# Kernel optimization log

Hardware: AMD Instinct MI355X
Metric: run time of the kernel (lower is better)

## Reference

```python
import jax, jax.numpy as jnp
import numpy as np

# model dims
B, L, D, K = 4, 1024, 512, 24      # batch, seq_len, d_model, num_eigh
KU, KY, NL, DT = 3, 2, 4, 512      # ar depth u, ar depth y, num_layers, d_target
EPS = 1e-5


def _hankel_eigh():
    # Hankel matrix Z[i,j] = 2 / ((i+j)^3 - (i+j)), i,j in 1..L; top-K eigenpairs
    idx = np.arange(1, L + 1, dtype=np.float64)
    s = idx[:, None] + idx[None, :]
    Z = 2.0 / (s ** 3 - s)
    vals, vecs = np.linalg.eigh(Z)  # ascending
    return (jnp.asarray(vals[-K:], jnp.float32),       # [K]
            jnp.asarray(vecs[:, -K:], jnp.float32))    # [L, K]


def setup_inputs() -> dict:
    key = jax.random.key(0)
    ks = jax.random.split(key, 12)
    sc = 1.0 / np.sqrt(D)
    eig_vals, eig_vecs = _hankel_eigh()
    return {
        "inputs": jax.random.normal(ks[0], (B, L, D), jnp.float32),
        "emb_w": jax.random.normal(ks[1], (D, D), jnp.float32) * sc,
        "emb_b": jnp.zeros((D,), jnp.float32),
        "ln_scale": jnp.ones((NL, D), jnp.float32),
        "ln_bias": jnp.zeros((NL, D), jnp.float32),
        "m_y": jax.random.normal(ks[2], (NL, D, KY, D), jnp.float32) * 0.02,
        "m_u": jax.random.normal(ks[3], (NL, D, D, KU), jnp.float32) * sc,
        "m_phi": jax.random.normal(ks[4], (NL, D * K, D), jnp.float32) * 0.02,
        "w1": jax.random.normal(ks[5], (NL, D, 2 * D), jnp.float32) * sc,
        "b1": jnp.zeros((NL, 2 * D), jnp.float32),
        "proj_w": jax.random.normal(ks[6], (D, DT), jnp.float32) * sc,
        "proj_b": jnp.zeros((DT,), jnp.float32),
        "eig_vals": eig_vals,
        "eig_vecs": eig_vecs,
    }


def _layer_norm(x, s, b):
    mu = jnp.mean(x, axis=-1, keepdims=True)
    var = jnp.mean(jnp.square(x - mu), axis=-1, keepdims=True)
    return (x - mu) * jax.lax.rsqrt(var + EPS) * s + b


def _stu(x, m_y_l, m_u_l, m_phi_l, eig_vals, eig_vecs):
    # x: [B, L, D]
    n = 2 * L
    U = jnp.fft.rfft(x, n=n, axis=1)                 # [B, nf, D]
    V = jnp.fft.rfft(eig_vecs, n=n, axis=0)          # [nf, K]
    # causal conv of each eigvec filter with each channel -> x_tilde [B, L, K, D]
    xt = jnp.fft.irfft(U[:, :, None, :] * V[None, :, :, None], n=n, axis=1)[:, :L]
    xt = xt * (eig_vals[None, None, :, None] ** 0.25)
    delta_phi = xt.reshape(B, L, K * D) @ m_phi_l    # [B, L, D]
    ar = jnp.zeros_like(delta_phi)
    for i in range(KU):
        c = jnp.einsum('bli,oi->blo', x, m_u_l[:, :, i])
        if i > 0:
            c = jnp.pad(c, ((0, 0), (i, 0), (0, 0)))[:, :L]
        ar = ar + c
    deltas = delta_phi + ar
    # y_t = sum_{j<KY} m_y[:,j,:] @ y_{t-1-j} + delta_t  (sequential recurrence)
    def step(carry, d_t):                            # carry [B, KY, D], d_t [B, D]
        y = jnp.einsum('okd,bkd->bo', m_y_l, carry) + d_t
        carry = jnp.concatenate([y[:, None, :], carry[:, :-1]], axis=1)
        return carry, y
    _, ys = jax.lax.scan(step, jnp.zeros((B, KY, D), x.dtype),
                         jnp.transpose(deltas, (1, 0, 2)))
    return jnp.transpose(ys, (1, 0, 2))              # [B, L, D]


def reference(inputs, emb_w, emb_b, ln_scale, ln_bias, m_y, m_u, m_phi,
              w1, b1, proj_w, proj_b, eig_vals, eig_vecs):
    x = inputs @ emb_w + emb_b
    for l in range(NL):
        z = x
        h = _layer_norm(x, ln_scale[l], ln_bias[l])
        h = _stu(h, m_y[l], m_u[l], m_phi[l], eig_vals, eig_vecs)
        h = jax.nn.gelu(h, approximate=False)        # torch GELU default (erf)
        g = h @ w1[l] + b1[l]
        a, b = jnp.split(g, 2, axis=-1)
        h = a * jax.nn.sigmoid(b)                    # GLU(dim=-1)
        x = h + z                                    # residual (dropout=0, eval)
    return x @ proj_w + proj_b
```

## Files before the change

### kernel.cpp

```cpp
#include <hip/hip_runtime.h>
#include <math.h>

typedef __bf16 bf;
typedef __attribute__((ext_vector_type(4))) __bf16 bfv4;
typedef __attribute__((ext_vector_type(8))) __bf16 bfv8;
typedef __attribute__((ext_vector_type(4))) float f32x4;

__device__ __forceinline__ void gload16(const void* g, void* l) {
  __builtin_amdgcn_global_load_lds((const __attribute__((address_space(1))) void*)g,
                                   (__attribute__((address_space(3))) void*)l, 16, 0, 0);
}

struct GOp {
  const bf* A; long la, lKa, lMa, sAz; int zshA, kzA;
  const bf* B; long lb, lKb, sBz; int zmskB, kzB;
  float* C; long ldc, sCz;
  bf* Cb; long ldcb, sCbz;
  const float* bias; int K, maskCmp, mBlk, spS;
};

template<int tB,int tF32,int tB16,int tMASK,int tACC>
__device__ __forceinline__ void gbody(const GOp g, int z, long m0, long n0,
                                      bf* lsA, bf* lsB, const bf* zpg) {
  const int t = threadIdx.x;
  const bf* Ap = g.A + (long)(z >> g.zshA) * g.sAz;
  const bf* Bp = g.B + (long)(z & g.zmskB) * g.sBz;
  const int w = t >> 6, l = t & 63;
  const int wm = (w >> 1) * 64, wn = (w & 1) * 64;
  const int lr = l & 15, lk = (l >> 4) * 8;
  const int r0 = t >> 2, ko = (t & 3) * 8;
  const long rowA1 = m0 + r0, rowA2 = rowA1 + 64;
  const long baseA1 = (rowA1 >> 9) * g.lMa + (rowA1 & 511) * g.la;
  const long baseA2 = (rowA2 >> 9) * g.lMa + (rowA2 & 511) * g.la;
  const long baseB1 = (n0 + r0) * g.lb;
  const int zbA = z * g.kzA, zbB = z * g.kzB;
  const int ct = ((int)rowA1 + 1) & 7;
  const long convB = (long)ct * 2065 + 1023 - (long)rowA1;
  f32x4 acc[4][4];
  #pragma unroll
  for (int i = 0; i < 4; i++)
    #pragma unroll
    for (int j = 0; j < 4; j++) acc[i][j] = (f32x4){0.f, 0.f, 0.f, 0.f};

  for (int k0 = 0; k0 < g.K; k0 += 32) {
    const int kk = k0 + ko;
    const int bA = (kk >> 9) + zbA, bB = (kk >> 9) + zbB;
    const long kb = (long)bB * g.lKb + (kk & 511);
    const bf* ga; const bf* ga2;
    if (tMASK == 3) {
      ga  = Ap + convB + kk;
      ga2 = ga - 64;
    } else {
      const long ka = (long)bA * g.lKa + (kk & 511);
      ga  = Ap + baseA1 + ka;
      ga2 = Ap + baseA2 + ka;
      if (tMASK == 1) { if ((int)(rowA1 & 15) < bA) { ga = zpg; ga2 = zpg; } }
      if (tMASK == 2) { if ((int)(rowA1 & 63) < g.maskCmp) { ga = zpg; ga2 = zpg; } }
    }
    const bf* gb = Bp + baseB1 + kb;
    gload16(ga,             &lsA[t * 8]);
    gload16(ga2,            &lsA[2048 + t * 8]);
    gload16(gb,             &lsB[t * 8]);
    gload16(gb + 64 * g.lb, &lsB[2048 + t * 8]);
    __syncthreads();
    bfv8 av[4], bv[4];
    #pragma unroll
    for (int i = 0; i < 4; i++) av[i] = *(const bfv8*)&lsA[(wm + i * 16 + lr) * 32 + lk];
    #pragma unroll
    for (int i = 0; i < 4; i++) bv[i] = *(const bfv8*)&lsB[(wn + i * 16 + lr) * 32 + lk];
    #pragma unroll
    for (int i = 0; i < 4; i++)
      #pragma unroll
      for (int j = 0; j < 4; j++)
        acc[i][j] = __builtin_amdgcn_mfma_f32_16x16x32_bf16(av[i], bv[j], acc[i][j], 0, 0, 0);
    __syncthreads();
  }
  const int orow = (l >> 4) * 4, ocol = lr;
  #pragma unroll
  for (int i = 0; i < 4; i++)
    #pragma unroll
    for (int j = 0; j < 4; j++) {
      long col = n0 + wn + j * 16 + ocol;
      float bb = tB ? g.bias[col] : 0.f;
      #pragma unroll
      for (int r = 0; r < 4; r++) {
        long row = m0 + wm + i * 16 + orow + r;
        float v = acc[i][j][r] + bb;
        if (tF32) {
          long idx = (long)z * g.sCz + row * g.ldc + col;
          if (tACC) v += g.C[idx];
          g.C[idx] = v;
        }
        if (tB16) g.Cb[(long)z * g.sCbz + row * g.ldcb + col] = (bf)v;
      }
    }
}

template<int tB,int tF32,int tB16,int tMASK,int tACC,int tSPEC=0,
         int sB=0,int sF32=0,int sB16=0,int sMASK=0,int sACC=0>
__global__ __launch_bounds__(256) void gemm_k(GOp g, GOp gx, GOp gy, int Zmain,
                                              const bf* __restrict__ zpg) {
  __shared__ bf lsA[4096], lsB[4096];
  int z = blockIdx.z;
  if (tSPEC && z >= Zmain) {
    int flat = (z - Zmain) * (int)(gridDim.x * gridDim.y)
             + (int)blockIdx.y * (int)gridDim.x + (int)blockIdx.x;
    if (flat >= gx.mBlk) return;
    int zz = flat >> 6, t64 = flat & 63;
    long m0 = (long)(t64 >> 3) * 128, n0 = (long)(t64 & 7) * 128;
    if (zz < gx.spS) gbody<sB,sF32,sB16,sMASK,sACC>(gx, zz, m0, n0, lsA, lsB, zpg);
    else             gbody<sB,sF32,sB16,sMASK,sACC>(gy, 0,  m0, n0, lsA, lsB, zpg);
  } else {
    gbody<tB,tF32,tB16,tMASK,tACC>(g, z, (long)blockIdx.x * 128, (long)blockIdx.y * 128,
                                   lsA, lsB, zpg);
  }
}

static inline GOp mkop(const void* A, long la, long lKa, long lMa, long sAz, int zshA, int kzA,
                       const void* B, long lb, long lKb, long sBz, int zmskB, int kzB,
                       void* C, long ldc, long sCz, void* Cb, long ldcb, long sCbz,
                       const void* bias, int K) {
  GOp g;
  g.A = (const bf*)A; g.la = la; g.lKa = lKa; g.lMa = lMa; g.sAz = sAz; g.zshA = zshA; g.kzA = kzA;
  g.B = (const bf*)B; g.lb = lb; g.lKb = lKb; g.sBz = sBz; g.zmskB = zmskB; g.kzB = kzB;
  g.C = (float*)C; g.ldc = ldc; g.sCz = sCz;
  g.Cb = (bf*)Cb; g.ldcb = ldcb; g.sCbz = sCbz;
  g.bias = (const float*)bias; g.K = K; g.maskCmp = 0; g.mBlk = 0; g.spS = 0;
  return g;
}

template<int tB,int tF32,int tB16,int tMASK,int tACC,int tSPEC=0,
         int sB=0,int sF32=0,int sB16=0,int sMASK=0,int sACC=0>
static inline void LG(hipStream_t st, int gx_, int gy_, int gz_, const GOp& g,
                      const GOp& gsx, const GOp& gsy, int Zmain, const bf* zpg) {
  gemm_k<tB,tF32,tB16,tMASK,tACC,tSPEC,sB,sF32,sB16,sMASK,sACC>
      <<<dim3(gx_, gy_, gz_), 256, 0, st>>>(g, gsx, gsy, Zmain, zpg);
}


template<typename TI, typename TO>
__global__ __launch_bounds__(256) void k_trt(const TI* __restrict__ in, TO* __restrict__ out,
                                             long ldin, long inz, long ldout, long outz) {
  __shared__ float tile[64][65];
  int z = blockIdx.z;
  int c0 = blockIdx.x * 64, r0 = blockIdx.y * 64;
  int tx = threadIdx.x & 63, ty = threadIdx.x >> 6;
  #pragma unroll
  for (int i = ty; i < 64; i += 4) tile[i][tx] = (float)in[(long)z * inz + (long)(c0 + i) * ldin + r0 + tx];
  __syncthreads();
  #pragma unroll
  for (int i = ty; i < 64; i += 4) out[(long)z * outz + (long)(r0 + i) * ldout + c0 + tx] = (TO)tile[tx][i];
}

__global__ __launch_bounds__(256) void k_trtS(const float* __restrict__ in, bf* __restrict__ out,
                                              long ldin, long ldout, const float* __restrict__ scl) {
  __shared__ float tile[64][65];
  int c0 = blockIdx.x * 64, r0 = blockIdx.y * 64;
  int tx = threadIdx.x & 63, ty = threadIdx.x >> 6;
  #pragma unroll
  for (int i = ty; i < 64; i += 4) tile[i][tx] = in[(long)(c0 + i) * ldin + r0 + tx];
  __syncthreads();
  float sc = scl[(c0 + tx) >> 9];
  #pragma unroll
  for (int i = ty; i < 64; i += 4) out[(long)(r0 + i) * ldout + c0 + tx] = (bf)(tile[tx][i] * sc);
}

__global__ void k_scl(const float* __restrict__ evals, float* __restrict__ scl) {
  int k = threadIdx.x;
  if (k < 24) scl[k] = powf(evals[k], 0.25f);
}

__global__ void k_pvec(const float* __restrict__ evecs, bf* __restrict__ out) {
  long id = (long)blockIdx.x * 256 + threadIdx.x;
  if (id >= 24L * 16512) return;
  int kf = (int)(id / 16512);
  int rem = (int)(id % 16512);
  int c = rem / 2064, j = rem % 2064;
  int d = j - c;
  float v = (d >= 0 && d <= 1023) ? evecs[(long)(1023 - d) * 24 + kf] : 0.f;
  out[id] = (bf)v;
}

__global__ void k_mut(const float* __restrict__ mul_, bf* __restrict__ out) {
  long id = (long)blockIdx.x * 256 + threadIdx.x;
  long r = id >> 9; int d = (int)(id & 511);
  int i = (int)(r >> 9), o = (int)(r & 511);
  out[id] = (bf)mul_[(long)o * 1536 + d * 3 + i];
}

__global__ __launch_bounds__(256) void k_prep(const float* __restrict__ myl,
                                              bf* __restrict__ cmpow, bf* __restrict__ trs) {
  __shared__ float t[64][65];
  long bid = blockIdx.x;
  if (bid < 10240) {
    long id = bid * 256 + threadIdx.x;
    if (id < 2097152) {
      int half = (int)(id >> 20);
      int r = (int)(id & 1048575);
      int p = r >> 10, q = r & 1023;
      float v;
      if (half == 0) v = (p == q) ? 1.f : 0.f;
      else if (p < 512) v = myl[(long)p * 1024 + q];
      else v = (q == p - 512) ? 1.f : 0.f;
      cmpow[id] = (bf)v;
    } else if (id < 2621440) {
      long id2 = id - 2097152;
      int x = (int)(id2 >> 9), y = (int)(id2 & 511);
      trs[(long)x * 1024 + 512 + y] = (bf)((x == y) ? 1.f : 0.f);
    }
  } else {
    int tile = (int)(bid - 10240);
    int txx = tile >> 3, tyy = tile & 7;
    int lx = threadIdx.x & 63, ly = threadIdx.x >> 6;
    #pragma unroll
    for (int i = ly; i < 64; i += 4)
      t[i][lx] = myl[(long)(tyy * 64 + i) * 1024 + txx * 64 + lx];
    __syncthreads();
    #pragma unroll
    for (int i = ly; i < 64; i += 4)
      trs[(long)(txx * 64 + i) * 1024 + tyy * 64 + lx] = (bf)t[lx][i];
  }
}

__global__ __launch_bounds__(256) void k_ln(const float* __restrict__ x, const float* __restrict__ sc,
                                            const float* __restrict__ bi, bf* __restrict__ hb) {
  __shared__ float red[8];
  long row = blockIdx.x;
  const float* xr = x + row * 512;
  int t = threadIdx.x;
  float a = xr[t], b2 = xr[t + 256];
  float s = a + b2;
  #pragma unroll
  for (int o = 32; o; o >>= 1) s += __shfl_down(s, o, 64);
  if ((t & 63) == 0) red[t >> 6] = s;
  __syncthreads();
  float mu = (red[0] + red[1] + red[2] + red[3]) * (1.f / 512.f);
  __syncthreads();
  float c1 = a - mu, c2 = b2 - mu;
  float qq = c1 * c1 + c2 * c2;
  #pragma unroll
  for (int o = 32; o; o >>= 1) qq += __shfl_down(qq, o, 64);
  if ((t & 63) == 0) red[t >> 6] = qq;
  __syncthreads();
  float var = (red[0] + red[1] + red[2] + red[3]) * (1.f / 512.f);
  float rs = rsqrtf(var + 1e-5f);
  hb[row * 512 + t]       = (bf)(c1 * rs * sc[t] + bi[t]);
  hb[row * 512 + t + 256] = (bf)(c2 * rs * sc[t + 256] + bi[t + 256]);
}

__global__ void k_deltasS(const float* __restrict__ dp, long stride, int S,
                          const bf* __restrict__ callb, bf* __restrict__ db) {
  long id = (long)blockIdx.x * 256 + threadIdx.x;
  int o = (int)(id & 511); long row = id >> 9; int tt = (int)(row & 1023);
  float v = 0.f;
  for (int zz = 0; zz < S; ++zz) v += dp[(long)zz * stride + id];
  for (int i = 0; i < 3; ++i)
    if (tt >= i) v += (float)callb[(row - i) * 1536 + i * 512 + o];
  db[id] = (bf)v;
}

__global__ void k_egather(const float* __restrict__ dp, long stride, int S,
                          float* __restrict__ E, bf* __restrict__ eb0) {
  long id = (long)blockIdx.x * 256 + threadIdx.x;
  int p = (int)(id & 1023); long r = id >> 10;
  int b = (int)(r >> 6), c = (int)(r & 63);
  int tq = c * 16 + ((p < 512) ? 15 : 14);
  long idx = ((long)(b << 10) + tq) * 512 + (p & 511);
  float v = 0.f;
  for (int zz = 0; zz < S; ++zz) v += dp[(long)zz * stride + idx];
  E[id] = v; eb0[id] = (bf)v;
}

__global__ void k_sfinal(const float* __restrict__ E, bf* __restrict__ ssb) {
  long id = (long)blockIdx.x * 256 + threadIdx.x;
  int c = (int)((id >> 10) & 63);
  ssb[id] = (c > 0) ? (bf)E[id - 1024] : (bf)0.f;
}

__global__ void k_combgelu(const float* __restrict__ dp, long stride, int S,
                           const bf* __restrict__ outh, bf* __restrict__ yg) {
  long id = (long)blockIdx.x * 256 + threadIdx.x;
  int o = (int)(id & 511); long row = id >> 9;
  int b = (int)(row >> 10), tt = (int)(row & 1023);
  int c = tt >> 4, j = tt & 15;
  long wv = ((long)(j * 512 + o)) * 256 + b * 64 + c;
  float v = (float)outh[wv];
  for (int zz = 0; zz < S; ++zz) v += dp[(long)zz * stride + id];
  yg[id] = (bf)(0.5f * v * (1.f + erff(v * 0.70710678118654752f)));
}

__global__ void k_glures(const bf* __restrict__ g, float* __restrict__ x) {
  long id = (long)blockIdx.x * 256 + threadIdx.x;
  int o = (int)(id & 511); long row = id >> 9;
  float a = (float)g[row * 1024 + o], bb = (float)g[row * 1024 + 512 + o];
  x[id] = x[id] + a / (1.f + expf(-bb));
}

__global__ void k_cast(const float* __restrict__ in, bf* __restrict__ out, long n4) {
  long id = (long)blockIdx.x * 256 + threadIdx.x;
  if (id >= n4) return;
  float4 v = *(const float4*)(in + id * 4);
  bfv4 o; o[0] = (bf)v.x; o[1] = (bf)v.y; o[2] = (bf)v.z; o[3] = (bf)v.w;
  *(bfv4*)(out + id * 4) = o;
}

__global__ void k_fill(float* p, long n, float v) {
  long id = (long)blockIdx.x * 256 + threadIdx.x;
  if (id < n) p[id] = v;
}

struct Lay {
  long ZPG, SSTB, SCL, EMBT, PROJT, PVEC, CMPOW, TRS, WU, X, MPHITL, MUTL, W1TL,
       HB, HTB, DSLOT, DP, RC, E, EB0, EB1, need;
  int nk, S;
};
static Lay mkLay(int nk, int S) {
  Lay L; long o = 0;
  auto al = [&](long sz) { long r = o; o += (sz + 255) & ~255L; return r; };
  L.nk = nk; L.S = S;
  L.ZPG   = al(4096);
  L.SSTB  = al(524288);
  L.SCL   = al(256);
  L.EMBT  = al(524288);
  L.PROJT = al(524288);
  L.PVEC  = al(24L * 16512 * 2);
  L.CMPOW = al(17L * 2097152);
  L.TRS   = al(2L * 2097152);
  L.WU    = al(8388608);
  L.X     = al(8388608);
  L.MPHITL= al(12582912);
  L.MUTL  = al(1572864);
  L.W1TL  = al(1048576);
  L.HB    = al(4194304);
  L.HTB   = al(4194304);
  L.DSLOT = al(4194304);
  L.DP    = al((long)S * 8388608);
  long rc = (long)nk * 4194304;
  if (rc < 16777216) rc = 16777216;
  L.RC    = al(rc);
  L.E     = al(1048576);
  L.EB0   = al(524288);
  L.EB1   = al(524288);
  L.need  = o;
  return L;
}

extern "C" void kernel_launch(void* const* d_in, const int* in_sizes, int n_in,
                              void* d_out, int out_size, void* d_ws, size_t ws_size,
                              hipStream_t stream) {
  Lay L = mkLay(12, 4);
  if (L.need > (long)ws_size) L = mkLay(8, 4);
  if (L.need > (long)ws_size) L = mkLay(4, 2);
  if (L.need > (long)ws_size) {
    k_fill<<<8192, 256, 0, stream>>>((float*)d_out, 2097152, 1.0e6f + (float)(ws_size >> 20));
    return;
  }
  const float* inp  = (const float*)d_in[0];
  const float* embw = (const float*)d_in[1];
  const float* embb = (const float*)d_in[2];
  const float* lns  = (const float*)d_in[3];
  const float* lnb  = (const float*)d_in[4];
  const float* m_y  = (const float*)d_in[5];
  const float* m_u  = (const float*)d_in[6];
  const float* mphi = (const float*)d_in[7];
  const float* w1   = (const float*)d_in[8];
  const float* b1   = (const float*)d_in[9];
  const float* pw   = (const float*)d_in[10];
  const float* pb   = (const float*)d_in[11];
  const float* evals = (const float*)d_in[12];
  const float* evecs = (const float*)d_in[13];

  char* w = (char*)d_ws;
  bf*    ZPG   = (bf*)(w + L.ZPG);
  bf*    SSTB  = (bf*)(w + L.SSTB);
  float* SCL   = (float*)(w + L.SCL);
  bf*    EMBT  = (bf*)(w + L.EMBT);
  bf*    PROJT = (bf*)(w + L.PROJT);
  bf*    PVEC  = (bf*)(w + L.PVEC);
  bf*    CMPOW = (bf*)(w + L.CMPOW);
  bf*    TRSa  = (bf*)(w + L.TRS);
  bf*    TRSb  = TRSa + 1048576;
  bf*    WUa   = (bf*)(w + L.WU);
  bf*    WUb   = (bf*)(w + L.WU + 4194304);
  float* X     = (float*)(w + L.X);
  bf*    MPHITL= (bf*)(w + L.MPHITL);
  bf*    MUTL  = (bf*)(w + L.MUTL);
  bf*    W1TL  = (bf*)(w + L.W1TL);
  bf*    HB    = (bf*)(w + L.HB);
  bf*    HTB   = (bf*)(w + L.HTB);
  bf*    DELTAB= (bf*)(w + L.DSLOT);
  bf*    YGB   = (bf*)(w + L.DSLOT);
  float* DP    = (float*)(w + L.DP);
  bf*    XTC   = (bf*)(w + L.RC);
  bf*    CALLB = (bf*)(w + L.RC);
  bf*    OUTH  = (bf*)(w + L.RC + 12582912);
  bf*    G     = (bf*)(w + L.RC);
  float* E     = (float*)(w + L.E);
  bf*    EB0   = (bf*)(w + L.EB0);
  bf*    EB1   = (bf*)(w + L.EB1);
  bf*    INB   = HB;
  hipStream_t st = stream;
  const int nk = L.nk, S = L.S, nchunk = 24 / nk;
  const long DPS = 2097152;
  const int Kcphi = nk * 512 / S, kzphi = Kcphi >> 9;
  const int Kcy = 8192 / S, kzy = Kcy >> 9;
  GOp gnull = {};
  const int BIGZ = 1 << 30;

  hipMemsetAsync(w + L.ZPG, 0, 4096, st);

  k_scl<<<1, 32, 0, st>>>(evals, SCL);
  k_pvec<<<1549, 256, 0, st>>>(evecs, PVEC);
  k_trt<float, bf><<<dim3(8, 8, 1), 256, 0, st>>>(embw, EMBT, 512, 0, 512, 0);
  k_trt<float, bf><<<dim3(8, 8, 1), 256, 0, st>>>(pw, PROJT, 512, 0, 512, 0);
  k_cast<<<2048, 256, 0, st>>>(inp, INB, 524288);
  LG<1,1,0,0,0>(st, 32, 4, 1,
      mkop(INB, 512, 512, 262144, 0, 30, 0, EMBT, 512, 512, 0, 0, 0,
           X, 512, 0, nullptr, 0, 0, embb, 512), gnull, gnull, BIGZ, ZPG);

  for (int l = 0; l < 4; ++l) {
    k_prep<<<10368, 256, 0, st>>>(m_y + (long)l * 524288, CMPOW, TRSa);
    k_trtS<<<dim3(192, 8, 1), 256, 0, st>>>(mphi + (long)l * 6291456, MPHITL, 512, 12288, SCL);
    k_mut<<<3072, 256, 0, st>>>(m_u + (long)l * 786432, MUTL);
    k_trt<float, bf><<<dim3(8, 16, 1), 256, 0, st>>>(w1 + (long)l * 524288, W1TL, 1024, 0, 512, 0);

    k_ln<<<4096, 256, 0, st>>>(X, lns + l * 512, lnb + l * 512, HB);
    k_trt<bf, bf><<<dim3(16, 8, 4), 256, 0, st>>>(HB, HTB, 512, 524288, 1024, 524288);

    int hostRound = 0;
    for (int kc = 0; kc < nchunk; ++kc) {
      GOp gconv = mkop(PVEC + (long)kc * nk * 16512, 0, 0, 0, 16512, 2, 0,
                       HTB, 1024, 512, 524288, 3, 0,
                       nullptr, 0, 0, XTC, 512, 524288, nullptr, 1024);
      if (hostRound < 4) {
        int s = 1 << hostRound;
        bf* TRScur = (hostRound & 1) ? TRSb : TRSa;
        bf* TRSnxt = (hostRound & 1) ? TRSa : TRSb;
        GOp dx = mkop(CMPOW + 1048576, 1024, 512, 524288, 1048576, 0, 0,
                      TRScur, 1024, 512, 0, 0, 0,
                      nullptr, 0, 0, CMPOW + (long)(s + 1) * 1048576, 1024, 1048576,
                      nullptr, 1024);
        dx.mBlk = 64 * (s + 1); dx.spS = s;
        GOp dy = mkop(TRScur, 1024, 512, 524288, 0, 0, 0,
                      CMPOW + (long)s * 1048576, 1024, 512, 0, 0, 0,
                      nullptr, 0, 0, TRSnxt, 1024, 0, nullptr, 1024);
        int nzs = (64 * (s + 1) + 31) / 32;
        LG<0,0,1,3,0, 1, 0,0,1,0,0>(st, 8, 4, 4 * nk + nzs, gconv, dx, dy, 4 * nk, ZPG);
        ++hostRound;
      } else {
        LG<0,0,1,3,0>(st, 8, 4, 4 * nk, gconv, gnull, gnull, BIGZ, ZPG);
      }
      GOp gphi = mkop(XTC, 512, 2097152, 262144, 0, 30, kzphi,
                      MPHITL + (long)kc * nk * 512, 12288, 512, 0, 0, kzphi,
                      DP, 512, DPS, nullptr, 0, 0, nullptr, Kcphi);
      if (hostRound < 4) {
        int s = 1 << hostRound;
        bf* TRScur = (hostRound & 1) ? TRSb : TRSa;
        bf* TRSnxt = (hostRound & 1) ? TRSa : TRSb;
        GOp dx = mkop(CMPOW + 1048576, 1024, 512, 524288, 1048576, 0, 0,
                      TRScur, 1024, 512, 0, 0, 0,
                      nullptr, 0, 0, CMPOW + (long)(s + 1) * 1048576, 1024, 1048576,
                      nullptr, 1024);
        dx.mBlk = 64 * (s + 1); dx.spS = s;
        GOp dy = mkop(TRScur, 1024, 512, 524288, 0, 0, 0,
                      CMPOW + (long)s * 1048576, 1024, 512, 0, 0, 0,
                      nullptr, 0, 0, TRSnxt, 1024, 0, nullptr, 1024);
        int nzs = (64 * (s + 1) + 127) / 128;
        if (kc == 0) LG<0,1,0,0,0, 1, 0,0,1,0,0>(st, 32, 4, S + nzs, gphi, dx, dy, S, ZPG);
        else         LG<0,1,0,0,1, 1, 0,0,1,0,0>(st, 32, 4, S + nzs, gphi, dx, dy, S, ZPG);
        ++hostRound;
      } else {
        if (kc == 0) LG<0,1,0,0,0>(st, 32, 4, S, gphi, gnull, gnull, BIGZ, ZPG);
        else         LG<0,1,0,0,1>(st, 32, 4, S, gphi, gnull, gnull, BIGZ, ZPG);
      }
    }

    LG<0,0,1,0,0>(st, 32, 12, 1,
        mkop(HB, 512, 512, 262144, 0, 30, 0, MUTL, 512, 512, 0, 0, 0,
             nullptr, 0, 0, CALLB, 1536, 0, nullptr, 512), gnull, gnull, BIGZ, ZPG);
    k_deltasS<<<8192, 256, 0, st>>>(DP, DPS, S, CALLB, DELTAB);

    LG<0,1,0,1,0>(st, 32, 4, S,
        mkop(DELTAB, 512, -512, 262144, 0, 30, kzy,
             CMPOW, 1024, 1048576, 0, 0, kzy,
             DP, 512, DPS, nullptr, 0, 0, nullptr, Kcy), gnull, gnull, BIGZ, ZPG);

    k_egather<<<1024, 256, 0, st>>>(DP, DPS, S, E, EB0);
    const bf* Wc = CMPOW + 16L * 1048576;
    const bf* Uc = TRSa;
    bf* EBc = EB0; bf* EBn = EB1;
    bf* WUn = WUa;
    for (int k = 1; k <= 5; ++k) {
      int sh = 1 << (k - 1);
      GOp mn = mkop(Wc, 1024, 512, 524288, (long)(Uc - Wc), 0, 0,
                    Uc, 1024, 512, (long)(Wc - Uc), 1, 0,
                    nullptr, 0, 0, WUn, 1024, 1048576, nullptr, 1024);
      GOp sp = mkop(EBc - (long)sh * 1024, 1024, 512, 524288, 0, 30, 0,
                    Wc, 1024, 512, 0, 0, 0,
                    E, 1024, 0, EBn, 1024, 0, nullptr, 1024);
      sp.maskCmp = sh; sp.mBlk = 16; sp.spS = 99;
      LG<0,0,1,0,0, 1, 0,1,1,2,1>(st, 8, 8, 3, mn, sp, gnull, 2, ZPG);
      Wc = WUn; Uc = WUn + 1048576;
      WUn = (k & 1) ? WUb : WUa;
      bf* tmp = EBc; EBc = EBn; EBn = tmp;
    }
    GOp fe = mkop(EBc - 32L * 1024, 1024, 512, 524288, 0, 30, 0,
                  Wc, 1024, 512, 0, 0, 0,
                  E, 1024, 0, nullptr, 0, 0, nullptr, 1024);
    fe.maskCmp = 32;
    LG<0,1,0,2,1>(st, 2, 8, 1, fe, gnull, gnull, BIGZ, ZPG);
    k_sfinal<<<1024, 256, 0, st>>>(E, SSTB);

    LG<0,0,1,0,0>(st, 64, 2, 1,
        mkop(CMPOW + 1048576, 1024, 512, 1048576, 0, 30, 0,
             SSTB, 1024, 512, 0, 0, 0,
             nullptr, 0, 0, OUTH, 256, 0, nullptr, 1024), gnull, gnull, BIGZ, ZPG);
    k_combgelu<<<8192, 256, 0, st>>>(DP, DPS, S, OUTH, YGB);
    LG<1,0,1,0,0>(st, 32, 8, 1,
        mkop(YGB, 512, 512, 262144, 0, 30, 0, W1TL, 512, 512, 0, 0, 0,
             nullptr, 0, 0, G, 1024, 0, b1 + (long)l * 1024, 512), gnull, gnull, BIGZ, ZPG);
    k_glures<<<8192, 256, 0, st>>>(G, X);
  }

  k_cast<<<2048, 256, 0, st>>>(X, INB, 524288);
  LG<1,1,0,0,0>(st, 32, 4, 1,
      mkop(INB, 512, 512, 262144, 0, 30, 0, PROJT, 512, 512, 0, 0, 0,
           (float*)d_out, 512, 0, nullptr, 0, 0, pb, 512), gnull, gnull, BIGZ, ZPG);
}
```

Before: 2.986 ms.

## Store only the top half of companion-matrix powers and trim triangular conv K-loop

Companion matrix powers are now stored as 512-row top halves (PTOP) with negative strides instead of full 1024x1024 blocks, because the bottom half is a shifted copy of the previous power. This halves both the power-doubling GEMM work and the memory traffic for the prep kernel. The Toeplitz conv GEMM (mask 3) now stops its K loop at m0+128, skipping the zero upper triangle. The last doubling step also drops the unused W-power grid slice. Together these rework the indexing across several GEMMs, so any addressing mistake would give wrong results.

```diff
diff --git a/kernel.cpp b/kernel.cpp
--- a/kernel.cpp
+++ b/kernel.cpp
@@ -36,13 +36,14 @@
   const int zbA = z * g.kzA, zbB = z * g.kzB;
   const int ct = ((int)rowA1 + 1) & 7;
   const long convB = (long)ct * 2065 + 1023 - (long)rowA1;
+  const int Kend = (tMASK == 3) ? ((g.K < (int)m0 + 128) ? g.K : (int)m0 + 128) : g.K;
   f32x4 acc[4][4];
   #pragma unroll
   for (int i = 0; i < 4; i++)
     #pragma unroll
     for (int j = 0; j < 4; j++) acc[i][j] = (f32x4){0.f, 0.f, 0.f, 0.f};
 
-  for (int k0 = 0; k0 < g.K; k0 += 32) {
+  for (int k0 = 0; k0 < Kend; k0 += 32) {
     const int kk = k0 + ko;
     const int bA = (kk >> 9) + zbA, bB = (kk >> 9) + zbB;
     const long kb = (long)bB * g.lKb + (kk & 511);
@@ -106,10 +107,16 @@
     int flat = (z - Zmain) * (int)(gridDim.x * gridDim.y)
              + (int)blockIdx.y * (int)gridDim.x + (int)blockIdx.x;
     if (flat >= gx.mBlk) return;
-    int zz = flat >> 6, t64 = flat & 63;
-    long m0 = (long)(t64 >> 3) * 128, n0 = (long)(t64 & 7) * 128;
-    if (zz < gx.spS) gbody<sB,sF32,sB16,sMASK,sACC>(gx, zz, m0, n0, lsA, lsB, zpg);
-    else             gbody<sB,sF32,sB16,sMASK,sACC>(gy, 0,  m0, n0, lsA, lsB, zpg);
+    int dxT = gx.spS * 32;
+    if (flat < dxT) {
+      int zz = flat >> 5, t32 = flat & 31;
+      gbody<sB,sF32,sB16,sMASK,sACC>(gx, zz, (long)(t32 >> 3) * 128, (long)(t32 & 7) * 128,
+                                     lsA, lsB, zpg);
+    } else {
+      int f = flat - dxT;
+      gbody<sB,sF32,sB16,sMASK,sACC>(gy, 0, (long)(f >> 3) * 128, (long)(f & 7) * 128,
+                                     lsA, lsB, zpg);
+    }
   } else {
     gbody<tB,tF32,tB16,tMASK,tACC>(g, z, (long)blockIdx.x * 128, (long)blockIdx.y * 128,
                                    lsA, lsB, zpg);
@@ -189,27 +196,28 @@
 }
 
 __global__ __launch_bounds__(256) void k_prep(const float* __restrict__ myl,
-                                              bf* __restrict__ cmpow, bf* __restrict__ trs) {
+                                              bf* __restrict__ ptop, bf* __restrict__ trs) {
   __shared__ float t[64][65];
   long bid = blockIdx.x;
-  if (bid < 10240) {
-    long id = bid * 256 + threadIdx.x;
-    if (id < 2097152) {
-      int half = (int)(id >> 20);
-      int r = (int)(id & 1048575);
-      int p = r >> 10, q = r & 1023;
-      float v;
-      if (half == 0) v = (p == q) ? 1.f : 0.f;
-      else if (p < 512) v = myl[(long)p * 1024 + q];
-      else v = (q == p - 512) ? 1.f : 0.f;
-      cmpow[id] = (bf)v;
-    } else if (id < 2621440) {
-      long id2 = id - 2097152;
-      int x = (int)(id2 >> 9), y = (int)(id2 & 511);
-      trs[(long)x * 1024 + 512 + y] = (bf)((x == y) ? 1.f : 0.f);
+  if (bid < 768) {
+    long id = bid * 2048 + (long)threadIdx.x * 8;
+    #pragma unroll
+    for (int u = 0; u < 8; ++u) {
+      long i = id + u;
+      if (i < 524288) {
+        ptop[15L * 524288 + i] = (bf)myl[i];
+      } else if (i < 1048576) {
+        long i2 = i - 524288;
+        int p = (int)(i2 >> 10), q = (int)(i2 & 1023);
+        ptop[16L * 524288 + i2] = (bf)((q == p) ? 1.f : 0.f);
+      } else {
+        long i3 = i - 1048576;
+        int x = (int)(i3 >> 9), y = (int)(i3 & 511);
+        trs[(long)x * 1024 + 512 + y] = (bf)((x == y) ? 1.f : 0.f);
+      }
     }
   } else {
-    int tile = (int)(bid - 10240);
+    int tile = (int)(bid - 768);
     int txx = tile >> 3, tyy = tile & 7;
     int lx = threadIdx.x & 63, ly = threadIdx.x >> 6;
     #pragma unroll
@@ -310,7 +318,7 @@
 }
 
 struct Lay {
-  long ZPG, SSTB, SCL, EMBT, PROJT, PVEC, CMPOW, TRS, WU, X, MPHITL, MUTL, W1TL,
+  long ZPG, SSTB, SCL, EMBT, PROJT, PVEC, PTOP, TRS, WU, X, MPHITL, MUTL, W1TL,
        HB, HTB, DSLOT, DP, RC, E, EB0, EB1, need;
   int nk, S;
 };
@@ -324,7 +332,7 @@
   L.EMBT  = al(524288);
   L.PROJT = al(524288);
   L.PVEC  = al(24L * 16512 * 2);
-  L.CMPOW = al(17L * 2097152);
+  L.PTOP  = al(17L * 1048576);
   L.TRS   = al(2L * 2097152);
   L.WU    = al(8388608);
   L.X     = al(8388608);
@@ -377,7 +385,7 @@
   bf*    EMBT  = (bf*)(w + L.EMBT);
   bf*    PROJT = (bf*)(w + L.PROJT);
   bf*    PVEC  = (bf*)(w + L.PVEC);
-  bf*    CMPOW = (bf*)(w + L.CMPOW);
+  bf*    PTOP  = (bf*)(w + L.PTOP);
   bf*    TRSa  = (bf*)(w + L.TRS);
   bf*    TRSb  = TRSa + 1048576;
   bf*    WUa   = (bf*)(w + L.WU);
@@ -419,7 +427,7 @@
            X, 512, 0, nullptr, 0, 0, embb, 512), gnull, gnull, BIGZ, ZPG);
 
   for (int l = 0; l < 4; ++l) {
-    k_prep<<<10368, 256, 0, st>>>(m_y + (long)l * 524288, CMPOW, TRSa);
+    k_prep<<<896, 256, 0, st>>>(m_y + (long)l * 524288, PTOP, TRSa);
     k_trtS<<<dim3(192, 8, 1), 256, 0, st>>>(mphi + (long)l * 6291456, MPHITL, 512, 12288, SCL);
     k_mut<<<3072, 256, 0, st>>>(m_u + (long)l * 786432, MUTL);
     k_trt<float, bf><<<dim3(8, 16, 1), 256, 0, st>>>(w1 + (long)l * 524288, W1TL, 1024, 0, 512, 0);
@@ -428,6 +436,16 @@
     k_trt<bf, bf><<<dim3(16, 8, 4), 256, 0, st>>>(HB, HTB, 512, 524288, 1024, 524288);
 
     int hostRound = 0;
+    auto mkDXY = [&](int s, bf* TRScur, bf* TRSnxt, GOp& dx, GOp& dy) {
+      dx = mkop(PTOP + 15L * 524288, 1024, 512, 0, -524288L, 0, 0,
+                TRScur, 1024, 512, 0, 0, 0,
+                nullptr, 0, 0, PTOP + (long)(15 - s) * 524288, 1024, -524288L,
+                nullptr, 1024);
+      dx.mBlk = 32 * s + 64; dx.spS = s;
+      dy = mkop(TRScur, 1024, 512, 524288, 0, 0, 0,
+                PTOP + (long)(16 - s) * 524288, 1024, 512, 0, 0, 0,
+                nullptr, 0, 0, TRSnxt, 1024, 0, nullptr, 1024);
+    };
     for (int kc = 0; kc < nchunk; ++kc) {
       GOp gconv = mkop(PVEC + (long)kc * nk * 16512, 0, 0, 0, 16512, 2, 0,
                        HTB, 1024, 512, 524288, 3, 0,
@@ -436,15 +454,8 @@
         int s = 1 << hostRound;
         bf* TRScur = (hostRound & 1) ? TRSb : TRSa;
         bf* TRSnxt = (hostRound & 1) ? TRSa : TRSb;
-        GOp dx = mkop(CMPOW + 1048576, 1024, 512, 524288, 1048576, 0, 0,
-                      TRScur, 1024, 512, 0, 0, 0,
-                      nullptr, 0, 0, CMPOW + (long)(s + 1) * 1048576, 1024, 1048576,
-                      nullptr, 1024);
-        dx.mBlk = 64 * (s + 1); dx.spS = s;
-        GOp dy = mkop(TRScur, 1024, 512, 524288, 0, 0, 0,
-                      CMPOW + (long)s * 1048576, 1024, 512, 0, 0, 0,
-                      nullptr, 0, 0, TRSnxt, 1024, 0, nullptr, 1024);
-        int nzs = (64 * (s + 1) + 31) / 32;
+        GOp dx, dy; mkDXY(s, TRScur, TRSnxt, dx, dy);
+        int nzs = (dx.mBlk + 31) / 32;
         LG<0,0,1,3,0, 1, 0,0,1,0,0>(st, 8, 4, 4 * nk + nzs, gconv, dx, dy, 4 * nk, ZPG);
         ++hostRound;
       } else {
@@ -457,15 +468,8 @@
         int s = 1 << hostRound;
         bf* TRScur = (hostRound & 1) ? TRSb : TRSa;
         bf* TRSnxt = (hostRound & 1) ? TRSa : TRSb;
-        GOp dx = mkop(CMPOW + 1048576, 1024, 512, 524288, 1048576, 0, 0,
-                      TRScur, 1024, 512, 0, 0, 0,
-                      nullptr, 0, 0, CMPOW + (long)(s + 1) * 1048576, 1024, 1048576,
-                      nullptr, 1024);
-        dx.mBlk = 64 * (s + 1); dx.spS = s;
-        GOp dy = mkop(TRScur, 1024, 512, 524288, 0, 0, 0,
-                      CMPOW + (long)s * 1048576, 1024, 512, 0, 0, 0,
-                      nullptr, 0, 0, TRSnxt, 1024, 0, nullptr, 1024);
-        int nzs = (64 * (s + 1) + 127) / 128;
+        GOp dx, dy; mkDXY(s, TRScur, TRSnxt, dx, dy);
+        int nzs = (dx.mBlk + 127) / 128;
         if (kc == 0) LG<0,1,0,0,0, 1, 0,0,1,0,0>(st, 32, 4, S + nzs, gphi, dx, dy, S, ZPG);
         else         LG<0,1,0,0,1, 1, 0,0,1,0,0>(st, 32, 4, S + nzs, gphi, dx, dy, S, ZPG);
         ++hostRound;
@@ -482,11 +486,11 @@
 
     LG<0,1,0,1,0>(st, 32, 4, S,
         mkop(DELTAB, 512, -512, 262144, 0, 30, kzy,
-             CMPOW, 1024, 1048576, 0, 0, kzy,
+             PTOP + 16L * 524288, 1024, -524288L, 0, 0, kzy,
              DP, 512, DPS, nullptr, 0, 0, nullptr, Kcy), gnull, gnull, BIGZ, ZPG);
 
     k_egather<<<1024, 256, 0, st>>>(DP, DPS, S, E, EB0);
-    const bf* Wc = CMPOW + 16L * 1048576;
+    const bf* Wc = PTOP;
     const bf* Uc = TRSa;
     bf* EBc = EB0; bf* EBn = EB1;
     bf* WUn = WUa;
@@ -499,7 +503,8 @@
                     Wc, 1024, 512, 0, 0, 0,
                     E, 1024, 0, EBn, 1024, 0, nullptr, 1024);
       sp.maskCmp = sh; sp.mBlk = 16; sp.spS = 99;
-      LG<0,0,1,0,0, 1, 0,1,1,2,1>(st, 8, 8, 3, mn, sp, gnull, 2, ZPG);
+      int gzN = (k < 5) ? 3 : 2, zm = (k < 5) ? 2 : 1;
+      LG<0,0,1,0,0, 1, 0,1,1,2,1>(st, 8, 8, gzN, mn, sp, gnull, zm, ZPG);
       Wc = WUn; Uc = WUn + 1048576;
       WUn = (k & 1) ? WUb : WUa;
       bf* tmp = EBc; EBc = EBn; EBn = tmp;
@@ -512,7 +517,7 @@
     k_sfinal<<<1024, 256, 0, st>>>(E, SSTB);
 
     LG<0,0,1,0,0>(st, 64, 2, 1,
-        mkop(CMPOW + 1048576, 1024, 512, 1048576, 0, 30, 0,
+        mkop(PTOP + 15L * 524288, 1024, 512, -524288L, 0, 30, 0,
              SSTB, 1024, 512, 0, 0, 0,
              nullptr, 0, 0, OUTH, 256, 0, nullptr, 1024), gnull, gnull, BIGZ, ZPG);
     k_combgelu<<<8192, 256, 0, st>>>(DP, DPS, S, OUTH, YGB);
```

Result: faster. 2.854 ms (-4.4%).
